# Kernel tuning notes

Hardware: AMD Instinct MI355X
Metric: run time of the kernel (lower is better)

## Reference

```python
import jax, jax.numpy as jnp
import numpy as np

B, T, S, R, D, F = 256, 8, 200, 8, 64, 20


def setup_inputs() -> dict:
    key = jax.random.key(0)
    ks = jax.random.split(key, 8)
    # 0.1 scale keeps attention logits in a reasonable range (like trained embeddings)
    seq = 0.1 * jax.random.normal(ks[0], (B, S, D), dtype=jnp.float32)
    delta_t_n = jax.random.uniform(ks[1], (B, S), dtype=jnp.float32)  # normalized time gaps
    target = 0.1 * jax.random.normal(ks[2], (B, T, D), dtype=jnp.float32)
    target_value = 0.1 * jax.random.normal(ks[3], (B, T, R, D), dtype=jnp.float32)
    valid_mask = jax.random.randint(ks[4], (B, 1, S, 1), 0, 2, dtype=jnp.int32)
    rel_emb = 0.1 * jax.random.normal(ks[5], (R, D), dtype=jnp.float32)
    freq_real = 0.1 * jax.random.normal(ks[6], (R, F), dtype=jnp.float32)
    freq_imag = 0.1 * jax.random.normal(ks[7], (R, F), dtype=jnp.float32)
    return dict(seq=seq, delta_t_n=delta_t_n, target=target, target_value=target_value,
                valid_mask=valid_mask, rel_emb=rel_emb, freq_real=freq_real, freq_imag=freq_imag)


def _idft_decay(delta_t_n, freq_real, freq_imag):
    # freqs: concat(linspace(0,1,F)/2, -linspace(0,1,F)/2) -> [2F]
    f = jnp.linspace(0.0, 1.0, F, dtype=jnp.float32) / 2.0
    freqs = jnp.concatenate([f, -f])
    x_real = jnp.concatenate([freq_real, freq_real], axis=-1)   # [R,2F]
    x_imag = jnp.concatenate([freq_imag, -freq_imag], axis=-1)  # [R,2F]
    w = 2.0 * jnp.pi * freqs * delta_t_n[..., None]             # [B,S,2F]
    # [B,S,1,2F] * [1,1,R,2F] -> mean over 2F -> [B,S,R]
    decay = (jnp.cos(w)[:, :, None, :] * x_real[None, None]
             - jnp.sin(w)[:, :, None, :] * x_imag[None, None]).mean(axis=-1) / 2.0
    return decay


def reference(seq, delta_t_n, target, target_value, valid_mask, rel_emb, freq_real, freq_imag):
    # include_val=True branch
    rv = rel_emb[None, None] + target_value              # [B,T,R,D]
    ri = rv * target[:, :, None, :]                      # [B,T,R,D]
    # scores: contraction over D, no [B,T,S,R,D] materialization
    att = jnp.einsum('bsd,btrd->btsr', seq, ri)          # [B,T,S,R]
    att = att - att.max()
    att = jnp.where(valid_mask == 0, -jnp.inf, att)
    att = jax.nn.softmax(att, axis=-2)                   # softmax over seq (S)
    decay = jnp.clip(_idft_decay(delta_t_n, freq_real, freq_imag), 0.0, 1.0)[:, None]  # [B,1,S,R]
    decay = jnp.where(valid_mask == 0, 0.0, decay)
    att = att * decay
    context = jnp.einsum('bsd,btsr->btrd', seq, att)     # [B,T,R,D]
    return context
```

## Files before the change

kernel.cpp:

```cpp
#include <hip/hip_runtime.h>
#include <math.h>

constexpr int kB = 256, kT = 8, kS = 200, kR = 8, kD = 64, kF = 20;
constexpr int TG = 4;

__global__ __launch_bounds__(256) void rda_fused(
    const float* __restrict__ seq,
    const float* __restrict__ dt,
    const float* __restrict__ target,
    const float* __restrict__ tv,
    const int*   __restrict__ vm,
    const float* __restrict__ rel,
    const float* __restrict__ fr,
    const float* __restrict__ fi,
    float* __restrict__ out)
{
    __shared__ float dec[kR][kS];
    __shared__ float ri[TG * kR * kD];
    __shared__ float att[TG][kR][kS];
    __shared__ float ff[2][kR][kF];

    const int o   = blockIdx.x;
    const int xcd = o & 7, q = o >> 3;
    const int tg  = q & 1;
    const int b   = xcd + 8 * (q >> 1);
    const int bt0 = b * kT + tg * TG;

    const int tid = threadIdx.x, wave = tid >> 6, lane = tid & 63;

    for (int idx = tid; idx < 2 * kR * kF; idx += 256)
        ((float*)ff)[idx] = (idx < kR * kF) ? fr[idx] : fi[idx - kR * kF];
    {
        const float* tvb = tv + (size_t)bt0 * kR * kD;
        const float* tgb = target + (size_t)bt0 * kD;
        for (int idx = tid; idx < TG * kR * kD; idx += 256) {
            int t = idx >> 9;
            ri[idx] = (rel[idx & 511] + tvb[idx]) * tgb[t * kD + (idx & 63)];
        }
    }
    __syncthreads();

    if (tid < kS) {
        const int s = tid;
        const bool valid = vm[b * kS + s] != 0;

        {
            const float t = dt[b * kS + s];
            float cs[kF], sn[kF];
#pragma unroll
            for (int k = 0; k < kF; ++k) {
                float fk = (float)k * (0.5f / (float)(kF - 1));
                sincosf(6.283185307179586f * fk * t, &sn[k], &cs[k]);
            }
#pragma unroll
            for (int r = 0; r < kR; ++r) {
                float acc = 0.f;
#pragma unroll
                for (int k = 0; k < kF; ++k)
                    acc += cs[k] * ff[0][r][k] - sn[k] * ff[1][r][k];
                acc *= (1.0f / (2.0f * (float)kF));
                acc = fminf(fmaxf(acc, 0.f), 1.f);
                dec[r][s] = valid ? acc : 0.f;
            }
        }

        {
            const float4* seqrow = (const float4*)(seq + (size_t)(b * kS + s) * kD);
            float a[TG][kR];
#pragma unroll
            for (int t = 0; t < TG; ++t)
#pragma unroll
                for (int r = 0; r < kR; ++r) a[t][r] = 0.f;
#pragma unroll
            for (int uu = 0; uu < kD / 4; ++uu) {
                float4 sv = seqrow[uu];
#pragma unroll
                for (int t = 0; t < TG; ++t)
#pragma unroll
                    for (int r = 0; r < kR; ++r) {
                        float4 rv = ((const float4*)(ri + (t * kR + r) * kD))[uu];
                        a[t][r] += sv.x * rv.x + sv.y * rv.y + sv.z * rv.z + sv.w * rv.w;
                    }
            }
#pragma unroll
            for (int t = 0; t < TG; ++t)
#pragma unroll
                for (int r = 0; r < kR; ++r)
                    att[t][r][s] = valid ? a[t][r] : -INFINITY;
        }
    }
    __syncthreads();

#pragma unroll
    for (int r = 0; r < kR; ++r) {
        float* row = &att[wave][r][0];
        float a0 = row[lane];
        float a1 = row[lane + 64];
        float a2 = row[lane + 128];
        float a3 = (lane < kS - 192) ? row[lane + 192] : -INFINITY;
        float m = fmaxf(fmaxf(a0, a1), fmaxf(a2, a3));
#pragma unroll
        for (int off = 32; off; off >>= 1) m = fmaxf(m, __shfl_xor(m, off));
        float e0 = __expf(a0 - m), e1 = __expf(a1 - m), e2 = __expf(a2 - m);
        float e3 = (lane < kS - 192) ? __expf(a3 - m) : 0.f;
        float ssum = e0 + e1 + e2 + e3;
#pragma unroll
        for (int off = 32; off; off >>= 1) ssum += __shfl_xor(ssum, off);
        const float inv = 1.0f / ssum;
        row[lane]       = e0 * inv * dec[r][lane];
        row[lane + 64]  = e1 * inv * dec[r][lane + 64];
        row[lane + 128] = e2 * inv * dec[r][lane + 128];
        if (lane < kS - 192)
            row[lane + 192] = e3 * inv * dec[r][lane + 192];
    }

    {
        float acc[kR];
#pragma unroll
        for (int r = 0; r < kR; ++r) acc[r] = 0.f;
        const float* seqb = seq + (size_t)b * kS * kD + lane;
        for (int s0 = 0; s0 < kS; s0 += 4) {
            float4 av[kR];
#pragma unroll
            for (int r = 0; r < kR; ++r)
                av[r] = *(const float4*)&att[wave][r][s0];
            float sv0 = seqb[(size_t)(s0 + 0) * kD];
            float sv1 = seqb[(size_t)(s0 + 1) * kD];
            float sv2 = seqb[(size_t)(s0 + 2) * kD];
            float sv3 = seqb[(size_t)(s0 + 3) * kD];
#pragma unroll
            for (int r = 0; r < kR; ++r)
                acc[r] += sv0 * av[r].x + sv1 * av[r].y + sv2 * av[r].z + sv3 * av[r].w;
        }
        float* ob = out + (size_t)(bt0 + wave) * kR * kD;
#pragma unroll
        for (int r = 0; r < kR; ++r)
            ob[r * kD + lane] = acc[r];
    }
}

extern "C" void kernel_launch(void* const* d_in, const int* in_sizes, int n_in,
                              void* d_out, int out_size, void* d_ws, size_t ws_size,
                              hipStream_t stream) {
    const float* seq    = (const float*)d_in[0];
    const float* dt     = (const float*)d_in[1];
    const float* target = (const float*)d_in[2];
    const float* tv     = (const float*)d_in[3];
    const int*   vm     = (const int*)  d_in[4];
    const float* rel    = (const float*)d_in[5];
    const float* fr     = (const float*)d_in[6];
    const float* fi     = (const float*)d_in[7];
    float* out = (float*)d_out;

    rda_fused<<<kB * (kT / TG), 256, 0, stream>>>(seq, dt, target, tv, vm, rel, fr, fi, out);
}
```

Before: 112.0 us.

## Split work to one block per (batch,target) with cross-wave S reduction

Each block now handles a single (b,t) pair instead of four targets, which quadruples the grid. Inside a block, the softmax rows are spread across waves and the context sum over S is split across the four waves, then combined through a shared-memory reduction. The decay now uses fast __sincosf with transposed frequency tables held in an aliased shared buffer, and launch bounds ask for higher occupancy. The cost is that the decay and the seq loads are recomputed for every target rather than shared across four, and there is an extra reduction step with added barriers.

```diff
diff --git a/kernel.cpp b/kernel.cpp
--- a/kernel.cpp
+++ b/kernel.cpp
@@ -2,9 +2,8 @@
 #include <math.h>
 
 constexpr int kB = 256, kT = 8, kS = 200, kR = 8, kD = 64, kF = 20;
-constexpr int TG = 4;
 
-__global__ __launch_bounds__(256) void rda_fused(
+__global__ __launch_bounds__(256, 8) void rda_fused(
     const float* __restrict__ seq,
     const float* __restrict__ dt,
     const float* __restrict__ target,
@@ -15,28 +14,35 @@
     const float* __restrict__ fi,
     float* __restrict__ out)
 {
-    __shared__ float dec[kR][kS];
-    __shared__ float ri[TG * kR * kD];
-    __shared__ float att[TG][kR][kS];
-    __shared__ float ff[2][kR][kF];
+    __shared__ float ri[kR * kD];
+    __shared__ float att[kR][kS];
+    __shared__ float u[2240];
 
-    const int o   = blockIdx.x;
-    const int xcd = o & 7, q = o >> 3;
-    const int tg  = q & 1;
-    const int b   = xcd + 8 * (q >> 1);
-    const int bt0 = b * kT + tg * TG;
-
+    const int o = blockIdx.x;
+    const int b = o & 255, t = o >> 8;
+    const int bt = b * kT + t;
     const int tid = threadIdx.x, wave = tid >> 6, lane = tid & 63;
 
-    for (int idx = tid; idx < 2 * kR * kF; idx += 256)
-        ((float*)ff)[idx] = (idx < kR * kF) ? fr[idx] : fi[idx - kR * kF];
+    float* dec = u;
+    float* frT = u + 1600;
+    float* fiT = u + 1760;
+    float* part = u;
+
+    if (tid < 2 * kR * kF) {
+        int idx = tid;
+        int tab = idx >= kR * kF; int j = idx - tab * kR * kF;
+        u[1600 + idx] = (tab ? fi : fr)[(j & 7) * kF + (j >> 3)];
+    }
+    if (tid < 2 * kR * kF - 256) {
+        int idx = tid + 256;
+        int j = idx - kR * kF;
+        u[1600 + idx] = fi[(j & 7) * kF + (j >> 3)];
+    }
     {
-        const float* tvb = tv + (size_t)bt0 * kR * kD;
-        const float* tgb = target + (size_t)bt0 * kD;
-        for (int idx = tid; idx < TG * kR * kD; idx += 256) {
-            int t = idx >> 9;
-            ri[idx] = (rel[idx & 511] + tvb[idx]) * tgb[t * kD + (idx & 63)];
-        }
+        const float* tvb = tv + (size_t)bt * kR * kD;
+        const float* tgb = target + (size_t)bt * kD;
+        for (int idx = tid; idx < kR * kD; idx += 256)
+            ri[idx] = (rel[idx] + tvb[idx]) * tgb[idx & 63];
     }
     __syncthreads();
 
@@ -45,55 +51,55 @@
         const bool valid = vm[b * kS + s] != 0;
 
         {
-            const float t = dt[b * kS + s];
-            float cs[kF], sn[kF];
+            const float tt = dt[b * kS + s];
+            float acc[kR];
+#pragma unroll
+            for (int r = 0; r < kR; ++r) acc[r] = 0.f;
 #pragma unroll
             for (int k = 0; k < kF; ++k) {
-                float fk = (float)k * (0.5f / (float)(kF - 1));
-                sincosf(6.283185307179586f * fk * t, &sn[k], &cs[k]);
+                float w = 6.283185307179586f * ((float)k * (0.5f / (kF - 1))) * tt;
+                float sn, cs; __sincosf(w, &sn, &cs);
+                float4 f0 = *(const float4*)&frT[k * 8];
+                float4 f1 = *(const float4*)&frT[k * 8 + 4];
+                float4 g0 = *(const float4*)&fiT[k * 8];
+                float4 g1 = *(const float4*)&fiT[k * 8 + 4];
+                acc[0] += cs * f0.x - sn * g0.x;  acc[1] += cs * f0.y - sn * g0.y;
+                acc[2] += cs * f0.z - sn * g0.z;  acc[3] += cs * f0.w - sn * g0.w;
+                acc[4] += cs * f1.x - sn * g1.x;  acc[5] += cs * f1.y - sn * g1.y;
+                acc[6] += cs * f1.z - sn * g1.z;  acc[7] += cs * f1.w - sn * g1.w;
             }
 #pragma unroll
             for (int r = 0; r < kR; ++r) {
-                float acc = 0.f;
-#pragma unroll
-                for (int k = 0; k < kF; ++k)
-                    acc += cs[k] * ff[0][r][k] - sn[k] * ff[1][r][k];
-                acc *= (1.0f / (2.0f * (float)kF));
-                acc = fminf(fmaxf(acc, 0.f), 1.f);
-                dec[r][s] = valid ? acc : 0.f;
+                float v = fminf(fmaxf(acc[r] * (1.0f / (2.0f * kF)), 0.f), 1.f);
+                dec[r * kS + s] = valid ? v : 0.f;
             }
         }
 
         {
             const float4* seqrow = (const float4*)(seq + (size_t)(b * kS + s) * kD);
-            float a[TG][kR];
+            float a[kR];
 #pragma unroll
-            for (int t = 0; t < TG; ++t)
-#pragma unroll
-                for (int r = 0; r < kR; ++r) a[t][r] = 0.f;
+            for (int r = 0; r < kR; ++r) a[r] = 0.f;
 #pragma unroll
             for (int uu = 0; uu < kD / 4; ++uu) {
                 float4 sv = seqrow[uu];
 #pragma unroll
-                for (int t = 0; t < TG; ++t)
-#pragma unroll
-                    for (int r = 0; r < kR; ++r) {
-                        float4 rv = ((const float4*)(ri + (t * kR + r) * kD))[uu];
-                        a[t][r] += sv.x * rv.x + sv.y * rv.y + sv.z * rv.z + sv.w * rv.w;
-                    }
+                for (int r = 0; r < kR; ++r) {
+                    float4 rv = ((const float4*)(ri + r * kD))[uu];
+                    a[r] += sv.x * rv.x + sv.y * rv.y + sv.z * rv.z + sv.w * rv.w;
+                }
             }
 #pragma unroll
-            for (int t = 0; t < TG; ++t)
-#pragma unroll
-                for (int r = 0; r < kR; ++r)
-                    att[t][r][s] = valid ? a[t][r] : -INFINITY;
+            for (int r = 0; r < kR; ++r)
+                att[r][s] = valid ? a[r] : -INFINITY;
         }
     }
     __syncthreads();
 
 #pragma unroll
-    for (int r = 0; r < kR; ++r) {
-        float* row = &att[wave][r][0];
+    for (int h = 0; h < 2; ++h) {
+        const int r = 2 * wave + h;
+        float* row = &att[r][0];
         float a0 = row[lane];
         float a1 = row[lane + 64];
         float a2 = row[lane + 128];
@@ -107,23 +113,25 @@
 #pragma unroll
         for (int off = 32; off; off >>= 1) ssum += __shfl_xor(ssum, off);
         const float inv = 1.0f / ssum;
-        row[lane]       = e0 * inv * dec[r][lane];
-        row[lane + 64]  = e1 * inv * dec[r][lane + 64];
-        row[lane + 128] = e2 * inv * dec[r][lane + 128];
+        row[lane]       = e0 * inv * dec[r * kS + lane];
+        row[lane + 64]  = e1 * inv * dec[r * kS + lane + 64];
+        row[lane + 128] = e2 * inv * dec[r * kS + lane + 128];
         if (lane < kS - 192)
-            row[lane + 192] = e3 * inv * dec[r][lane + 192];
+            row[lane + 192] = e3 * inv * dec[r * kS + lane + 192];
     }
+    __syncthreads();
 
     {
         float acc[kR];
 #pragma unroll
         for (int r = 0; r < kR; ++r) acc[r] = 0.f;
         const float* seqb = seq + (size_t)b * kS * kD + lane;
-        for (int s0 = 0; s0 < kS; s0 += 4) {
+        for (int g = wave; g < kS / 4; g += 4) {
+            const int s0 = 4 * g;
             float4 av[kR];
 #pragma unroll
             for (int r = 0; r < kR; ++r)
-                av[r] = *(const float4*)&att[wave][r][s0];
+                av[r] = *(const float4*)&att[r][s0];
             float sv0 = seqb[(size_t)(s0 + 0) * kD];
             float sv1 = seqb[(size_t)(s0 + 1) * kD];
             float sv2 = seqb[(size_t)(s0 + 2) * kD];
@@ -132,10 +140,19 @@
             for (int r = 0; r < kR; ++r)
                 acc[r] += sv0 * av[r].x + sv1 * av[r].y + sv2 * av[r].z + sv3 * av[r].w;
         }
-        float* ob = out + (size_t)(bt0 + wave) * kR * kD;
 #pragma unroll
         for (int r = 0; r < kR; ++r)
-            ob[r * kD + lane] = acc[r];
+            part[(wave * kR + r) * kD + lane] = acc[r];
+    }
+    __syncthreads();
+
+    {
+        int idx = tid;
+#pragma unroll
+        for (int it = 0; it < 2; ++it, idx += 256) {
+            float v = part[idx] + part[512 + idx] + part[1024 + idx] + part[1536 + idx];
+            out[(size_t)bt * kR * kD + idx] = v;
+        }
     }
 }
 
@@ -152,5 +169,5 @@
     const float* fi     = (const float*)d_in[7];
     float* out = (float*)d_out;
 
-    rda_fused<<<kB * (kT / TG), 256, 0, stream>>>(seq, dt, target, tv, vm, rel, fr, fi, out);
+    rda_fused<<<kB * kT, 256, 0, stream>>>(seq, dt, target, tv, vm, rel, fr, fi, out);
 }
```

Measured after the change: 297.8 us. +165.8%, slower.
